# Kernel tuning notes

Hardware: AMD Instinct MI355X
Metric: run time of the kernel (lower is better)

## Reference

```python
import jax, jax.numpy as jnp
import numpy as np
from functools import partial

H = 64  # hidden_size
F = 5   # num_features
ALPHA_RANK = 1.0
NEG_SLOPE = 0.2


def setup_inputs() -> dict:
    key = jax.random.key(0)
    ks = jax.random.split(key, 10)
    N, T = 4096, 512
    feature = jax.random.normal(ks[0], (N, T, F), dtype=jnp.float32)
    ret = jax.random.normal(ks[1], (N,), dtype=jnp.float32)
    mask = jax.random.bernoulli(ks[2], 0.9, (N,))
    s = 1.0 / np.sqrt(H)
    Wih = jax.random.uniform(ks[3], (4 * H, F), jnp.float32, -s, s)
    Whh = jax.random.uniform(ks[4], (4 * H, H), jnp.float32, -s, s)
    bih = jax.random.uniform(ks[5], (4 * H,), jnp.float32, -s, s)
    bhh = jax.random.uniform(ks[6], (4 * H,), jnp.float32, -s, s)
    Wd = jax.random.uniform(ks[7], (1, H), jnp.float32, -s, s)
    bd = jax.random.uniform(ks[8], (1,), jnp.float32, -s, s)
    return {"feature": feature, "ret": ret, "mask": mask,
            "Wih": Wih, "Whh": Whh, "bih": bih, "bhh": bhh,
            "Wd": Wd, "bd": bd}


def _lstm_last_h(x, Wih, Whh, bih, bhh):
    # x: [N, T, F] -> last hidden state [N, H]. PyTorch gate order: i, f, g, o.
    N = x.shape[0]
    b = bih + bhh
    # precompute input projections for all steps: [T, N, 4H]
    x_proj = jnp.einsum('ntf,gf->tng', x, Wih) + b

    def step(carry, xt):
        h, c = carry
        gates = xt + h @ Whh.T  # [N, 4H]
        i, f, g, o = jnp.split(gates, 4, axis=-1)
        i = jax.nn.sigmoid(i)
        f = jax.nn.sigmoid(f)
        g = jnp.tanh(g)
        o = jax.nn.sigmoid(o)
        c = f * c + i * g
        h = o * jnp.tanh(c)
        return (h, c), None

    h0 = jnp.zeros((N, H), x.dtype)
    c0 = jnp.zeros((N, H), x.dtype)
    (h, _), _ = jax.lax.scan(step, (h0, c0), x_proj)
    return h


def _masked_mse(pred, gt, mask):
    m = mask.astype(pred.dtype)
    return jnp.sum((pred - gt) ** 2 * m) / (jnp.sum(m) + 1e-8)


def _rank_loss(pred, gt, mask):
    m = mask.astype(pred.dtype)
    pred_diff = pred[None, :] - pred[:, None]   # [i,j] = pred[j]-pred[i]
    true_diff = gt[None, :] - gt[:, None]
    mm = m[None, :] * m[:, None]
    return jnp.mean(jax.nn.relu(-pred_diff * true_diff * mm))


def reference(feature, ret, mask, Wih, Whh, bih, bhh, Wd, bd):
    h_last = _lstm_last_h(feature, Wih, Whh, bih, bhh)          # [N, H]
    pred = jax.nn.leaky_relu(h_last @ Wd.T + bd, NEG_SLOPE)[:, 0]  # [N]
    reg_loss = _masked_mse(pred, ret, mask)
    rank_loss = _rank_loss(pred, ret, mask)
    loss = reg_loss + ALPHA_RANK * rank_loss
    return pred, loss, reg_loss, rank_loss
```

## Files before the change

### kernel.cpp

```cpp
#include <hip/hip_runtime.h>

#define NSEQ   4096
#define TSTEPS 512
#define FIN    5
#define HID    64
#define SPB    16
#define BLK    512

typedef __attribute__((ext_vector_type(8))) short bsh8;
typedef __attribute__((ext_vector_type(4))) float f32x4;
typedef __attribute__((ext_vector_type(4))) int   i32x4;

#define MFMA16(A, B, C) __builtin_amdgcn_mfma_f32_16x16x32_bf16((A), (B), (C), 0, 0, 0)

#define LOG2E 1.4426950408889634f
#define SNEG  (-LOG2E)
#define SPOS  (2.0f * LOG2E)

struct Frag2 { bsh8 hi; bsh8 lo; };

__device__ __forceinline__ unsigned short bf16hi_rn(float x) {
    unsigned u = __float_as_uint(x);
    return (unsigned short)((u + 0x7fffu + ((u >> 16) & 1u)) >> 16);
}
__device__ __forceinline__ void split_bf16(float v, unsigned short& h, unsigned short& l) {
    h = bf16hi_rn(v);
    float hf_ = __uint_as_float(((unsigned)h) << 16);
    l = bf16hi_rn(v - hf_);
}

__device__ __forceinline__ Frag2 load_whh_frag(const float* __restrict__ Whh, int row, int k, float scale) {
    const float* p = Whh + row * HID + k;
    Frag2 r;
#pragma unroll
    for (int j = 0; j < 8; ++j) {
        unsigned short h, l;
        split_bf16(scale * p[j], h, l);
        r.hi[j] = (short)h; r.lo[j] = (short)l;
    }
    return r;
}
__device__ __forceinline__ Frag2 load_wih_frag(const float* __restrict__ Wih,
                                               const float* __restrict__ bih,
                                               const float* __restrict__ bhh,
                                               int row, int quad, float scale) {
    Frag2 r;
#pragma unroll
    for (int j = 0; j < 8; ++j) { r.hi[j] = 0; r.lo[j] = 0; }
    if (quad == 0) {
        unsigned short h, l;
#pragma unroll
        for (int j = 0; j < FIN; ++j) {
            split_bf16(scale * Wih[row * FIN + j], h, l);
            r.hi[j] = (short)h; r.lo[j] = (short)l;
        }
        split_bf16(scale * (bih[row] + bhh[row]), h, l);
        r.hi[FIN] = (short)h; r.lo[FIN] = (short)l;
    }
    return r;
}

__device__ __forceinline__ void stage_chunk(const float* __restrict__ feat,
                                            bsh8 (*dst)[SPB],
                                            int seq0, int t0, int tidE) {
#pragma unroll
    for (int it = 0; it < (64 * SPB) / 256; ++it) {
        int idx = tidE + it * 256;
        int t2  = idx >> 4;
        int s   = idx & 15;
        const float* xp = feat + (size_t)(seq0 + s) * (TSTEPS * FIN) + (t0 + t2) * FIN;
        bsh8 v = {0, 0, 0, 0, 0, 0, 0, 0};
#pragma unroll
        for (int j = 0; j < FIN; ++j) v[j] = (short)bf16hi_rn(xp[j]);
        v[FIN] = (short)0x3F80;
        dst[t2][s] = v;
    }
}

__global__ __launch_bounds__(BLK)
void lstm_kernel(const float* __restrict__ feat,
                 const float* __restrict__ Wih,
                 const float* __restrict__ Whh,
                 const float* __restrict__ bih,
                 const float* __restrict__ bhh,
                 const float* __restrict__ Wd,
                 const float* __restrict__ bd,
                 float* __restrict__ pred,
                 float* __restrict__ accums) {
    __shared__ bsh8  aA[2][SPB][9];
    __shared__ bsh8  xb[2][64][SPB];
    __shared__ __align__(16) f32x4 seedb[2][4][4][64];
    __shared__ float hf[SPB][HID + 1];
    __shared__ float pf[SPB][17];

    const int tid   = threadIdx.x;
    const int w     = tid >> 6;
    const int lane  = tid & 63;
    const int col   = lane & 15;
    const int quad  = lane >> 4;
    const int quad4 = quad * 4;
    const int seq0  = blockIdx.x * SPB;

    if (blockIdx.x == 0 && tid < 4) accums[tid] = 0.0f;

    {
        bsh8 z = {0, 0, 0, 0, 0, 0, 0, 0};
        if (tid < SPB * 9) (&aA[0][0][0])[tid] = z;
    }
    if (w >= 4) stage_chunk(feat, xb[0], seq0, 0, tid - 256);
    __syncthreads();

    if (w < 4) {
        const int u = 16 * w + col;
        const Frag2 b00 = load_whh_frag(Whh, 0*HID + u,      quad*8, SNEG);
        const Frag2 b01 = load_whh_frag(Whh, 0*HID + u, 32 + quad*8, SNEG);
        const Frag2 b10 = load_whh_frag(Whh, 1*HID + u,      quad*8, SNEG);
        const Frag2 b11 = load_whh_frag(Whh, 1*HID + u, 32 + quad*8, SNEG);
        const Frag2 b20 = load_whh_frag(Whh, 2*HID + u,      quad*8, SPOS);
        const Frag2 b21 = load_whh_frag(Whh, 2*HID + u, 32 + quad*8, SPOS);
        const Frag2 b30 = load_whh_frag(Whh, 3*HID + u,      quad*8, SNEG);
        const Frag2 b31 = load_whh_frag(Whh, 3*HID + u, 32 + quad*8, SNEG);

        float cs_[4] = {0.f, 0.f, 0.f, 0.f};
        __builtin_amdgcn_s_setprio(1);

        for (int t = 0; t < TSTEPS; ++t) {
            const int buf = t & 1;
            const int nb  = buf ^ 1;
            __syncthreads();

            bsh8 ah0 = aA[buf][col][quad];
            bsh8 ah1 = aA[buf][col][4 + quad];
            f32x4 s0 = seedb[buf][w][0][lane];
            f32x4 s1 = seedb[buf][w][1][lane];
            f32x4 s2 = seedb[buf][w][2][lane];
            f32x4 s3 = seedb[buf][w][3][lane];

            const f32x4 zz = {0.f, 0.f, 0.f, 0.f};
            f32x4 acc0 = MFMA16(ah0, b00.hi, zz);
            f32x4 acc1 = MFMA16(ah0, b10.hi, zz);
            f32x4 acc2 = MFMA16(ah0, b20.hi, zz);
            f32x4 acc3 = MFMA16(ah0, b30.hi, zz);
            acc0 = MFMA16(ah1, b01.hi, acc0);
            acc1 = MFMA16(ah1, b11.hi, acc1);
            acc2 = MFMA16(ah1, b21.hi, acc2);
            acc3 = MFMA16(ah1, b31.hi, acc3);
            acc0 = MFMA16(ah0, b00.lo, acc0);
            acc1 = MFMA16(ah0, b10.lo, acc1);
            acc2 = MFMA16(ah0, b20.lo, acc2);
            acc3 = MFMA16(ah0, b30.lo, acc3);
            acc0 = MFMA16(ah1, b01.lo, acc0);
            acc1 = MFMA16(ah1, b11.lo, acc1);
            acc2 = MFMA16(ah1, b21.lo, acc2);
            acc3 = MFMA16(ah1, b31.lo, acc3);
            acc0 = acc0 + s0;
            acc1 = acc1 + s1;
            acc2 = acc2 + s2;
            acc3 = acc3 + s3;

            float hh_[4];
#pragma unroll
            for (int r = 0; r < 4; ++r) {
                float Ei = __builtin_amdgcn_exp2f(acc0[r]);
                float Ef = __builtin_amdgcn_exp2f(acc1[r]);
                float Eg = __builtin_amdgcn_exp2f(acc2[r]);
                float Eo = __builtin_amdgcn_exp2f(acc3[r]);
                float R1 = __builtin_amdgcn_rcpf((1.0f + Ei) * (1.0f + Eg));
                float sf = __builtin_amdgcn_rcpf(1.0f + Ef);
                float n1 = __builtin_fmaf(SPOS, Eg, -SPOS);
                cs_[r] = __builtin_fmaf(sf, cs_[r], n1 * R1);
                float Ec = __builtin_amdgcn_exp2f(cs_[r]);
                float R2 = __builtin_amdgcn_rcpf((1.0f + Eo) * (1.0f + Ec));
                hh_[r] = (Ec - 1.0f) * R2;
            }
            unsigned pk01, pk23;
            asm("v_cvt_pk_bf16_f32 %0, %1, %2" : "=v"(pk01) : "v"(hh_[0]), "v"(hh_[1]));
            asm("v_cvt_pk_bf16_f32 %0, %1, %2" : "=v"(pk23) : "v"(hh_[2]), "v"(hh_[3]));
            unsigned short* hp = (unsigned short*)&aA[nb][quad4][0] + u;
            hp[0]   = (unsigned short)pk01;
            hp[72]  = (unsigned short)(pk01 >> 16);
            hp[144] = (unsigned short)pk23;
            hp[216] = (unsigned short)(pk23 >> 16);
            if (t == TSTEPS - 1) {
                hf[quad4 + 0][u] = hh_[0];
                hf[quad4 + 1][u] = hh_[1];
                hf[quad4 + 2][u] = hh_[2];
                hf[quad4 + 3][u] = hh_[3];
            }
        }
        __builtin_amdgcn_s_setprio(0);
    } else {
        const int wE   = w - 4;
        const int tidE = tid - 256;
        const int uE   = 16 * wE + col;
        const Frag2 w0 = load_wih_frag(Wih, bih, bhh, 0*HID + uE, quad, SNEG);
        const Frag2 w1 = load_wih_frag(Wih, bih, bhh, 1*HID + uE, quad, SNEG);
        const Frag2 w2 = load_wih_frag(Wih, bih, bhh, 2*HID + uE, quad, SPOS);
        const Frag2 w3 = load_wih_frag(Wih, bih, bhh, 3*HID + uE, quad, SNEG);

        {
            bsh8 ax = xb[0][0][col];
            f32x4 e0 = {0.f,0.f,0.f,0.f}, e1 = e0, e2 = e0, e3 = e0;
            e0 = MFMA16(ax, w0.hi, e0); e0 = MFMA16(ax, w0.lo, e0);
            e1 = MFMA16(ax, w1.hi, e1); e1 = MFMA16(ax, w1.lo, e1);
            e2 = MFMA16(ax, w2.hi, e2); e2 = MFMA16(ax, w2.lo, e2);
            e3 = MFMA16(ax, w3.hi, e3); e3 = MFMA16(ax, w3.lo, e3);
            seedb[0][wE][0][lane] = e0;
            seedb[0][wE][1][lane] = e1;
            seedb[0][wE][2][lane] = e2;
            seedb[0][wE][3][lane] = e3;
        }
        for (int t = 0; t < TSTEPS; ++t) {
            __syncthreads();
            if ((t & 63) == 0 && t + 64 < TSTEPS)
                stage_chunk(feat, xb[((t >> 6) + 1) & 1], seq0, ((t >> 6) + 1) * 64, tidE);
            if (t + 1 < TSTEPS) {
                const int t1 = t + 1;
                bsh8 ax = xb[(t1 >> 6) & 1][t1 & 63][col];
                f32x4 e0 = {0.f,0.f,0.f,0.f}, e1 = e0, e2 = e0, e3 = e0;
                e0 = MFMA16(ax, w0.hi, e0); e0 = MFMA16(ax, w0.lo, e0);
                e1 = MFMA16(ax, w1.hi, e1); e1 = MFMA16(ax, w1.lo, e1);
                e2 = MFMA16(ax, w2.hi, e2); e2 = MFMA16(ax, w2.lo, e2);
                e3 = MFMA16(ax, w3.hi, e3); e3 = MFMA16(ax, w3.lo, e3);
                const int sb = t1 & 1;
                seedb[sb][wE][0][lane] = e0;
                seedb[sb][wE][1][lane] = e1;
                seedb[sb][wE][2][lane] = e2;
                seedb[sb][wE][3][lane] = e3;
            }
        }
    }
    __syncthreads();

    if (tid < 256) {
        int s  = tid & 15;
        int hq = tid >> 4;
        int j0 = hq * 4;
        float part = hf[s][j0] * Wd[j0] + hf[s][j0 + 1] * Wd[j0 + 1]
                   + hf[s][j0 + 2] * Wd[j0 + 2] + hf[s][j0 + 3] * Wd[j0 + 3];
        pf[s][hq] = part;
    }
    __syncthreads();
    if (tid < SPB) {
        float sum = bd[0];
#pragma unroll
        for (int j = 0; j < 16; ++j) sum += pf[tid][j];
        float p = (sum >= 0.0f) ? sum : 0.2f * sum;
        pred[seq0 + tid] = p;
    }
}

__global__ __launch_bounds__(256)
void loss_kernel(const float* __restrict__ pred,
                 const float* __restrict__ ret,
                 const int* __restrict__ mask,
                 float* __restrict__ accums) {
    __shared__ __align__(16) float sp[NSEQ];
    __shared__ __align__(16) float sg[NSEQ];
    __shared__ __align__(16) float sq[NSEQ];
    __shared__ float wsum[8];
    int tid = threadIdx.x;
    for (int idx = tid; idx < NSEQ / 4; idx += 256) {
        f32x4 p4 = ((const f32x4*)pred)[idx];
        f32x4 g4 = ((const f32x4*)ret)[idx];
        i32x4 m4 = ((const i32x4*)mask)[idx];
        f32x4 q4;
#pragma unroll
        for (int l = 0; l < 4; ++l) q4[l] = m4[l] ? 1.0f : 0.0f;
        *(f32x4*)&sp[idx * 4] = p4;
        *(f32x4*)&sg[idx * 4] = g4;
        *(f32x4*)&sq[idx * 4] = q4;
    }
    __syncthreads();

    if (blockIdx.x == 0) {
        float v = 0.0f, m = 0.0f;
        for (int j = tid; j < NSEQ; j += 256) {
            float mj = sq[j];
            float d  = sp[j] - sg[j];
            v += d * d * mj;
            m += mj;
        }
#pragma unroll
        for (int off = 32; off > 0; off >>= 1) {
            v += __shfl_down(v, off, 64);
            m += __shfl_down(m, off, 64);
        }
        if ((tid & 63) == 0) {
            atomicAdd(&accums[0], v);
            atomicAdd(&accums[1], m);
        }
    }

    int iloc = tid >> 5;
    int jp   = tid & 31;
    int i    = blockIdx.x * 8 + iloc;
    float pi = sp[i], gi = sg[i], qi = sq[i];
    float sum = 0.0f;
    for (int j0 = jp * 4; j0 < NSEQ; j0 += 128) {
        f32x4 p4 = *(const f32x4*)&sp[j0];
        f32x4 g4 = *(const f32x4*)&sg[j0];
        f32x4 q4 = *(const f32x4*)&sq[j0];
#pragma unroll
        for (int l = 0; l < 4; ++l) {
            float t = -(p4[l] - pi) * (g4[l] - gi);
            sum += fmaxf(t, 0.0f) * q4[l];
        }
    }
    sum *= qi;
#pragma unroll
    for (int off = 16; off > 0; off >>= 1) sum += __shfl_down(sum, off, 32);
    if (jp == 0) wsum[iloc] = sum;
    __syncthreads();
    if (tid == 0) {
        float s = wsum[0] + wsum[1] + wsum[2] + wsum[3]
                + wsum[4] + wsum[5] + wsum[6] + wsum[7];
        atomicAdd(&accums[2], s);
    }
}

__global__ void final_kernel(const float* __restrict__ accums,
                             float* __restrict__ out) {
    float reg  = accums[0] / (accums[1] + 1e-8f);
    float rank = accums[2] / 16777216.0f;
    out[NSEQ + 0] = reg + rank;
    out[NSEQ + 1] = reg;
    out[NSEQ + 2] = rank;
}

extern "C" void kernel_launch(void* const* d_in, const int* in_sizes, int n_in,
                              void* d_out, int out_size, void* d_ws, size_t ws_size,
                              hipStream_t stream) {
    const float* feat = (const float*)d_in[0];
    const float* ret  = (const float*)d_in[1];
    const int*   mask = (const int*)d_in[2];
    const float* Wih  = (const float*)d_in[3];
    const float* Whh  = (const float*)d_in[4];
    const float* bih  = (const float*)d_in[5];
    const float* bhh  = (const float*)d_in[6];
    const float* Wd   = (const float*)d_in[7];
    const float* bd   = (const float*)d_in[8];
    float* out    = (float*)d_out;
    float* accums = (float*)d_ws;

    lstm_kernel<<<NSEQ / SPB, BLK, 0, stream>>>(feat, Wih, Whh, bih, bhh,
                                                Wd, bd, out, accums);
    loss_kernel<<<NSEQ / 8, 256, 0, stream>>>(out, ret, mask, accums);
    final_kernel<<<1, 1, 0, stream>>>(accums, out);
}
```

Before: 351.1 us.

## Share reciprocals across LSTM gate pairs, split MFMA chains, fuse final reduction

The recurrent epilogue now handles two rows at once and computes one reciprocal per pair instead of one per row, cutting the number of rcp instructions per step in the serial LSTM loop. The MFMA accumulation is split into two independent chains per gate, with the input-projection seed folded in as the initial accumulator, which shortens dependent MFMA latency. The final-loss kernel is removed: the last loss block, detected through an atomic counter, writes the losses, saving one kernel launch. Risks are precision loss in the combined reciprocal, since the product of four denominators can overflow or underflow, and a dependence on accums[3] being zeroed before each call.

Result: slower. 359.1 us (+2.3%).

```diff
diff --git a/kernel.cpp b/kernel.cpp
--- a/kernel.cpp
+++ b/kernel.cpp
@@ -6,6 +6,7 @@
 #define HID    64
 #define SPB    16
 #define BLK    512
+#define LOSSB  512
 
 typedef __attribute__((ext_vector_type(8))) short bsh8;
 typedef __attribute__((ext_vector_type(4))) float f32x4;
@@ -75,6 +76,31 @@
         v[FIN] = (short)0x3F80;
         dst[t2][s] = v;
     }
+}
+
+__device__ __forceinline__ void epi2(float zi0, float zf0, float zg0, float zo0,
+                                     float zi1, float zf1, float zg1, float zo1,
+                                     float& cs0, float& cs1, float& h0, float& h1) {
+    float Ei0 = __builtin_amdgcn_exp2f(zi0), Ei1 = __builtin_amdgcn_exp2f(zi1);
+    float Ef0 = __builtin_amdgcn_exp2f(zf0), Ef1 = __builtin_amdgcn_exp2f(zf1);
+    float Eg0 = __builtin_amdgcn_exp2f(zg0), Eg1 = __builtin_amdgcn_exp2f(zg1);
+    float P10 = (1.0f + Ei0) * (1.0f + Eg0), Pf0 = 1.0f + Ef0;
+    float P11 = (1.0f + Ei1) * (1.0f + Eg1), Pf1 = 1.0f + Ef1;
+    float D0 = P10 * Pf0, D1 = P11 * Pf1;
+    float Rp = __builtin_amdgcn_rcpf(D0 * D1);
+    float n10 = __builtin_fmaf(SPOS, Eg0, -SPOS);
+    float n11 = __builtin_fmaf(SPOS, Eg1, -SPOS);
+    float m0 = __builtin_fmaf(P10, cs0, n10 * Pf0);
+    float m1 = __builtin_fmaf(P11, cs1, n11 * Pf1);
+    cs0 = (Rp * D1) * m0;
+    cs1 = (Rp * D0) * m1;
+    float Eo0 = __builtin_amdgcn_exp2f(zo0), Eo1 = __builtin_amdgcn_exp2f(zo1);
+    float Ec0 = __builtin_amdgcn_exp2f(cs0), Ec1 = __builtin_amdgcn_exp2f(cs1);
+    float D20 = (1.0f + Eo0) * (1.0f + Ec0);
+    float D21 = (1.0f + Eo1) * (1.0f + Ec1);
+    float R2p = __builtin_amdgcn_rcpf(D20 * D21);
+    h0 = (Ec0 - 1.0f) * (R2p * D21);
+    h1 = (Ec1 - 1.0f) * (R2p * D20);
 }
 
 __global__ __launch_bounds__(BLK)
@@ -121,8 +147,12 @@
         const Frag2 b30 = load_whh_frag(Whh, 3*HID + u,      quad*8, SNEG);
         const Frag2 b31 = load_whh_frag(Whh, 3*HID + u, 32 + quad*8, SNEG);
 
-        float cs_[4] = {0.f, 0.f, 0.f, 0.f};
+        float cs0 = 0.f, cs1 = 0.f, cs2 = 0.f, cs3 = 0.f;
         __builtin_amdgcn_s_setprio(1);
+
+        unsigned short* const aAb = (unsigned short*)&aA[0][0][0];
+        const int rowbase = quad4 * 72 + u;
+        const int aAhalf  = SPB * 9 * 8;
 
         for (int t = 0; t < TSTEPS; ++t) {
             const int buf = t & 1;
@@ -137,55 +167,46 @@
             f32x4 s3 = seedb[buf][w][3][lane];
 
             const f32x4 zz = {0.f, 0.f, 0.f, 0.f};
-            f32x4 acc0 = MFMA16(ah0, b00.hi, zz);
-            f32x4 acc1 = MFMA16(ah0, b10.hi, zz);
-            f32x4 acc2 = MFMA16(ah0, b20.hi, zz);
-            f32x4 acc3 = MFMA16(ah0, b30.hi, zz);
-            acc0 = MFMA16(ah1, b01.hi, acc0);
-            acc1 = MFMA16(ah1, b11.hi, acc1);
-            acc2 = MFMA16(ah1, b21.hi, acc2);
-            acc3 = MFMA16(ah1, b31.hi, acc3);
-            acc0 = MFMA16(ah0, b00.lo, acc0);
-            acc1 = MFMA16(ah0, b10.lo, acc1);
-            acc2 = MFMA16(ah0, b20.lo, acc2);
-            acc3 = MFMA16(ah0, b30.lo, acc3);
-            acc0 = MFMA16(ah1, b01.lo, acc0);
-            acc1 = MFMA16(ah1, b11.lo, acc1);
-            acc2 = MFMA16(ah1, b21.lo, acc2);
-            acc3 = MFMA16(ah1, b31.lo, acc3);
-            acc0 = acc0 + s0;
-            acc1 = acc1 + s1;
-            acc2 = acc2 + s2;
-            acc3 = acc3 + s3;
-
-            float hh_[4];
-#pragma unroll
-            for (int r = 0; r < 4; ++r) {
-                float Ei = __builtin_amdgcn_exp2f(acc0[r]);
-                float Ef = __builtin_amdgcn_exp2f(acc1[r]);
-                float Eg = __builtin_amdgcn_exp2f(acc2[r]);
-                float Eo = __builtin_amdgcn_exp2f(acc3[r]);
-                float R1 = __builtin_amdgcn_rcpf((1.0f + Ei) * (1.0f + Eg));
-                float sf = __builtin_amdgcn_rcpf(1.0f + Ef);
-                float n1 = __builtin_fmaf(SPOS, Eg, -SPOS);
-                cs_[r] = __builtin_fmaf(sf, cs_[r], n1 * R1);
-                float Ec = __builtin_amdgcn_exp2f(cs_[r]);
-                float R2 = __builtin_amdgcn_rcpf((1.0f + Eo) * (1.0f + Ec));
-                hh_[r] = (Ec - 1.0f) * R2;
-            }
+            f32x4 p0 = MFMA16(ah0, b00.hi, s0);
+            f32x4 q0 = MFMA16(ah1, b01.hi, zz);
+            f32x4 p1 = MFMA16(ah0, b10.hi, s1);
+            f32x4 q1 = MFMA16(ah1, b11.hi, zz);
+            f32x4 p2 = MFMA16(ah0, b20.hi, s2);
+            f32x4 q2 = MFMA16(ah1, b21.hi, zz);
+            f32x4 p3 = MFMA16(ah0, b30.hi, s3);
+            f32x4 q3 = MFMA16(ah1, b31.hi, zz);
+            p0 = MFMA16(ah0, b00.lo, p0);
+            q0 = MFMA16(ah1, b01.lo, q0);
+            p1 = MFMA16(ah0, b10.lo, p1);
+            q1 = MFMA16(ah1, b11.lo, q1);
+            p2 = MFMA16(ah0, b20.lo, p2);
+            q2 = MFMA16(ah1, b21.lo, q2);
+            p3 = MFMA16(ah0, b30.lo, p3);
+            q3 = MFMA16(ah1, b31.lo, q3);
+            f32x4 z0 = p0 + q0;
+            f32x4 z1 = p1 + q1;
+            f32x4 z2 = p2 + q2;
+            f32x4 z3 = p3 + q3;
+
+            float h0, h1, h2, h3;
+            epi2(z0[0], z1[0], z2[0], z3[0], z0[1], z1[1], z2[1], z3[1],
+                 cs0, cs1, h0, h1);
+            epi2(z0[2], z1[2], z2[2], z3[2], z0[3], z1[3], z2[3], z3[3],
+                 cs2, cs3, h2, h3);
+
             unsigned pk01, pk23;
-            asm("v_cvt_pk_bf16_f32 %0, %1, %2" : "=v"(pk01) : "v"(hh_[0]), "v"(hh_[1]));
-            asm("v_cvt_pk_bf16_f32 %0, %1, %2" : "=v"(pk23) : "v"(hh_[2]), "v"(hh_[3]));
-            unsigned short* hp = (unsigned short*)&aA[nb][quad4][0] + u;
+            asm("v_cvt_pk_bf16_f32 %0, %1, %2" : "=v"(pk01) : "v"(h0), "v"(h1));
+            asm("v_cvt_pk_bf16_f32 %0, %1, %2" : "=v"(pk23) : "v"(h2), "v"(h3));
+            unsigned short* hp = aAb + nb * aAhalf + rowbase;
             hp[0]   = (unsigned short)pk01;
             hp[72]  = (unsigned short)(pk01 >> 16);
             hp[144] = (unsigned short)pk23;
             hp[216] = (unsigned short)(pk23 >> 16);
             if (t == TSTEPS - 1) {
-                hf[quad4 + 0][u] = hh_[0];
-                hf[quad4 + 1][u] = hh_[1];
-                hf[quad4 + 2][u] = hh_[2];
-                hf[quad4 + 3][u] = hh_[3];
+                hf[quad4 + 0][u] = h0;
+                hf[quad4 + 1][u] = h1;
+                hf[quad4 + 2][u] = h2;
+                hf[quad4 + 3][u] = h3;
             }
         }
         __builtin_amdgcn_s_setprio(0);
@@ -254,9 +275,10 @@
 void loss_kernel(const float* __restrict__ pred,
                  const float* __restrict__ ret,
                  const int* __restrict__ mask,
-                 float* __restrict__ accums) {
+                 float* __restrict__ accums,
+                 float* __restrict__ out) {
     __shared__ __align__(16) float sp[NSEQ];
-    __shared__ __align__(16) float sg[NSEQ];
+    __shared__ __align__(16) float sg_[NSEQ];
     __shared__ __align__(16) float sq[NSEQ];
     __shared__ float wsum[8];
     int tid = threadIdx.x;
@@ -268,7 +290,7 @@
 #pragma unroll
         for (int l = 0; l < 4; ++l) q4[l] = m4[l] ? 1.0f : 0.0f;
         *(f32x4*)&sp[idx * 4] = p4;
-        *(f32x4*)&sg[idx * 4] = g4;
+        *(f32x4*)&sg_[idx * 4] = g4;
         *(f32x4*)&sq[idx * 4] = q4;
     }
     __syncthreads();
@@ -277,7 +299,7 @@
         float v = 0.0f, m = 0.0f;
         for (int j = tid; j < NSEQ; j += 256) {
             float mj = sq[j];
-            float d  = sp[j] - sg[j];
+            float d  = sp[j] - sg_[j];
             v += d * d * mj;
             m += mj;
         }
@@ -295,11 +317,11 @@
     int iloc = tid >> 5;
     int jp   = tid & 31;
     int i    = blockIdx.x * 8 + iloc;
-    float pi = sp[i], gi = sg[i], qi = sq[i];
+    float pi = sp[i], gi = sg_[i], qi = sq[i];
     float sum = 0.0f;
     for (int j0 = jp * 4; j0 < NSEQ; j0 += 128) {
         f32x4 p4 = *(const f32x4*)&sp[j0];
-        f32x4 g4 = *(const f32x4*)&sg[j0];
+        f32x4 g4 = *(const f32x4*)&sg_[j0];
         f32x4 q4 = *(const f32x4*)&sq[j0];
 #pragma unroll
         for (int l = 0; l < 4; ++l) {
@@ -316,16 +338,19 @@
         float s = wsum[0] + wsum[1] + wsum[2] + wsum[3]
                 + wsum[4] + wsum[5] + wsum[6] + wsum[7];
         atomicAdd(&accums[2], s);
-    }
-}
-
-__global__ void final_kernel(const float* __restrict__ accums,
-                             float* __restrict__ out) {
-    float reg  = accums[0] / (accums[1] + 1e-8f);
-    float rank = accums[2] / 16777216.0f;
-    out[NSEQ + 0] = reg + rank;
-    out[NSEQ + 1] = reg;
-    out[NSEQ + 2] = rank;
+        __threadfence();
+        float old = atomicAdd(&accums[3], 1.0f);
+        if (old == (float)(LOSSB - 1)) {
+            float a0 = atomicAdd(&accums[0], 0.0f);
+            float a1 = atomicAdd(&accums[1], 0.0f);
+            float a2 = atomicAdd(&accums[2], 0.0f);
+            float reg  = a0 / (a1 + 1e-8f);
+            float rank = a2 / 16777216.0f;
+            out[NSEQ + 0] = reg + rank;
+            out[NSEQ + 1] = reg;
+            out[NSEQ + 2] = rank;
+        }
+    }
 }
 
 extern "C" void kernel_launch(void* const* d_in, const int* in_sizes, int n_in,
@@ -345,6 +370,5 @@
 
     lstm_kernel<<<NSEQ / SPB, BLK, 0, stream>>>(feat, Wih, Whh, bih, bhh,
                                                 Wd, bd, out, accums);
-    loss_kernel<<<NSEQ / 8, 256, 0, stream>>>(out, ret, mask, accums);
-    final_kernel<<<1, 1, 0, stream>>>(accums, out);
-}
+    loss_kernel<<<LOSSB, 256, 0, stream>>>(out, ret, mask, accums, out);
+}
```
